# Performance work log

Hardware: AMD Instinct MI355X
Metric: run time of the kernel (lower is better)

Reference implementation:

```python
import jax, jax.numpy as jnp
import numpy as np

K = 8          # opt.pk, explicit precision cutoff
MARGIN = 0.2   # opt.margin
NEG = -1e30    # sentinel for masked sort keys


def setup_inputs() -> dict:
    key = jax.random.key(0)
    k1, k2 = jax.random.split(key)
    batch_reprs = jax.random.normal(k1, (4096, 512), dtype=jnp.float32)
    batch_labels = jax.random.randint(k2, (4096,), 0, 64)
    return {"batch_reprs": batch_reprs, "batch_labels": batch_labels}


def _forward(batch_reprs, batch_labels):
    B = batch_reprs.shape[0]
    dt = batch_reprs.dtype
    # cls_match_mat: 1 if same class
    match = (batch_labels[:, None] == batch_labels[None, :]).astype(dt)
    # pairwise euclidean distance (squared=False), safe sqrt at zero diagonal
    sq = jnp.sum(batch_reprs * batch_reprs, axis=1)
    res = jnp.maximum(sq[:, None] - 2.0 * (batch_reprs @ batch_reprs.T) + sq[None, :], 0.0)
    zero = res <= 0.0
    d = jnp.where(zero, 0.0, jnp.sqrt(jnp.where(zero, 1.0, res)))
    sim_hat = -d + (1.0 - match) * MARGIN  # use_margin=True path
    # rank via double argsort (descending similarity -> rank 1 = best)
    order = jnp.argsort(-sim_hat, axis=1)
    rank = jnp.argsort(order, axis=1).astype(dt) + 1.0
    pos_nums = jnp.sum(match, axis=1)
    ks = jnp.minimum(pos_nums, jnp.asarray(K + 1, dt))[:, None]  # k_mat per row
    w = 1.0 / jnp.log2(rank + 1.0) + 1.0  # DCG-style rank weight
    # false positives: not same class, within top-k_i
    fp_mask = (match < 1.0) & (rank <= ks)
    fp_nums = jnp.sum(fp_mask, axis=1)  # |N| per row
    # false negatives: same class, beyond top-k_i
    fn_mask = (match > 0.0) & (rank > ks)
    fp_term = jnp.sum(jnp.where(fp_mask, sim_hat * w, 0.0))
    # per-row variable-size topk over false negatives, vectorized:
    # mask non-FN entries to -inf, sort desc, keep first fp_nums[i] entries
    fn_key = jnp.where(fn_mask, sim_hat, NEG)
    fn_order = jnp.argsort(-fn_key, axis=1)
    sorted_sim = jnp.take_along_axis(sim_hat, fn_order, axis=1)
    sorted_w = jnp.take_along_axis(w, fn_order, axis=1)
    sorted_valid = jnp.take_along_axis(fn_mask, fn_order, axis=1)
    take = (jnp.arange(B)[None, :].astype(dt) < fp_nums[:, None]) & sorted_valid
    fn_term = jnp.sum(jnp.where(take, sorted_sim * sorted_w, 0.0))
    # rows with fp_num==0 contribute 0 to both terms, matching the host loop
    return fp_term - fn_term


def reference(batch_reprs, batch_labels):
    return _forward(batch_reprs, batch_labels)
```

## Files before the change

kernel.cpp:

```cpp
#include <hip/hip_runtime.h>
#include <math.h>

#define BB 4096
#define DD 512
#define KTOP 9
#define MARGIN_F 0.2f
#define NT64 64
#define NTRI64 (NT64 * (NT64 + 1) / 2)

typedef __attribute__((ext_vector_type(8))) short short8;
typedef __attribute__((ext_vector_type(4))) float f32x4;
typedef unsigned long long u64;

__device__ unsigned short g_Rhi[(size_t)BB * DD];
__device__ u64 g_cmask[64 * 64];

__device__ __forceinline__ unsigned short f2bf(float x) {
  unsigned u = __float_as_uint(x);
  u += 0x7fffu + ((u >> 16) & 1u);
  return (unsigned short)(u >> 16);
}

__device__ __forceinline__ void gload16(void* lds, const void* g) {
  __builtin_amdgcn_global_load_lds(
      (const __attribute__((address_space(1))) void*)g,
      (__attribute__((address_space(3))) void*)lds, 16, 0, 0);
}

__device__ __forceinline__ float ord16val(unsigned o16) {
  unsigned e = (o16 << 16) | 0x8000u;
  unsigned s = (e & 0x80000000u) ? (e ^ 0x80000000u) : ~e;
  return __uint_as_float(s);
}

__device__ __forceinline__ unsigned wavemax32_dpp(unsigned c) {
#define MSTEP(CTRL, RM)                                                        \
  {                                                                            \
    unsigned o = (unsigned)__builtin_amdgcn_update_dpp(0, (int)c, CTRL, RM, 0xf, false); \
    if (o > c) c = o;                                                          \
  }
  MSTEP(0xB1, 0xf) MSTEP(0x4E, 0xf) MSTEP(0x141, 0xf) MSTEP(0x140, 0xf)
  MSTEP(0x142, 0xa) MSTEP(0x143, 0xc)
#undef MSTEP
  return (unsigned)__builtin_amdgcn_readlane((int)c, 63);
}

__device__ __forceinline__ int wavesum_dpp(int c) {
#define SSTEP(CTRL, RM)                                                        \
  c += __builtin_amdgcn_update_dpp(0, c, CTRL, RM, 0xf, false);
  SSTEP(0xB1, 0xf) SSTEP(0x4E, 0xf) SSTEP(0x141, 0xf) SSTEP(0x140, 0xf)
  SSTEP(0x142, 0xa) SSTEP(0x143, 0xc)
#undef SSTEP
  return __builtin_amdgcn_readlane(c, 63);
}

__device__ __forceinline__ unsigned u4c(const uint4& f, int q) {
  return q == 0 ? f.x : q == 1 ? f.y : q == 2 ? f.z : f.w;
}

__global__ __launch_bounds__(64) void splitsq(const float* __restrict__ R,
                                              float* __restrict__ sq) {
  const int row = blockIdx.x, lane = threadIdx.x;
  const float4* r4 = (const float4*)(R + (size_t)row * DD);
  float4 a = r4[lane], b = r4[lane + 64];
  float xs[8] = {a.x, a.y, a.z, a.w, b.x, b.y, b.z, b.w};
  unsigned short hs[8];
  float s = 0.f;
  #pragma unroll
  for (int q = 0; q < 8; ++q) {
    float x = xs[q];
    s += x * x;
    hs[q] = f2bf(x);
  }
  const size_t base = (size_t)row * DD;
  *(ushort4*)&g_Rhi[base + lane * 4]       = *(ushort4*)&hs[0];
  *(ushort4*)&g_Rhi[base + 256 + lane * 4] = *(ushort4*)&hs[4];
  #pragma unroll
  for (int off = 32; off; off >>= 1) s += __shfl_down(s, off);
  if (lane == 0) sq[row] = s;
}

__global__ __launch_bounds__(64) void buildmask(const int* __restrict__ labels) {
  __shared__ int slab[BB];
  const int c = blockIdx.x, lane = threadIdx.x;
  for (int i = lane; i < BB / 4; i += 64) ((int4*)slab)[i] = ((const int4*)labels)[i];
  __syncthreads();
  u64 m = 0;
  #pragma unroll
  for (int e = 0; e < 64; ++e) {
    int j = 512 * (e >> 3) + 8 * lane + (e & 7);
    m |= (u64)(slab[j] == c) << e;
  }
  g_cmask[c * 64 + lane] = m;
}

__global__ __launch_bounds__(64) void simgemm_wave(const int* __restrict__ labels,
                                                   const float* __restrict__ sq,
                                                   unsigned short* __restrict__ simq) {
  const int x = blockIdx.x & 7;
  int c = blockIdx.x >> 3;
  int bi = 0, bj = 0;
  #pragma unroll
  for (int q = 0; q < 8; ++q) {
    const int bjq = (q < 4) ? (4 * x + q) : (56 - 4 * x + q);
    const int n = bjq + 1;
    if (c >= 0 && c < n) { bj = bjq; bi = c; }
    c -= n;
  }
  const int i0 = bi * 64, j0 = bj * 64;

  __shared__ unsigned short smem[2][2][2048];

  const int lane = threadIdx.x;
  const int lrow = lane & 15, kblk = lane >> 4;

  f32x4 acc[4][4] = {};

  auto stage = [&](int buf, int k0) {
    const int sr = lane & 15;
    const int sc = (lane >> 4) * 8;
    #pragma unroll
    for (int m = 0; m < 4; ++m) {
      gload16(&smem[buf][0][m * 512], &g_Rhi[(size_t)(i0 + m * 16 + sr) * DD + k0 + sc]);
      gload16(&smem[buf][1][m * 512], &g_Rhi[(size_t)(j0 + m * 16 + sr) * DD + k0 + sc]);
    }
  };

  stage(0, 0);
  stage(1, 32);

  #pragma unroll
  for (int step = 0; step < 16; ++step) {
    const int cur = step & 1;
    if (step == 15) asm volatile("s_waitcnt vmcnt(0)" ::: "memory");
    else            asm volatile("s_waitcnt vmcnt(8)" ::: "memory");
    __builtin_amdgcn_sched_barrier(0);

    short8 a[4], b[4];
    #pragma unroll
    for (int m = 0; m < 4; ++m) a[m] = *(const short8*)&smem[cur][0][m * 512 + lane * 8];
    #pragma unroll
    for (int n = 0; n < 4; ++n) b[n] = *(const short8*)&smem[cur][1][n * 512 + lane * 8];
    asm volatile("s_waitcnt lgkmcnt(0)" ::: "memory");
    __builtin_amdgcn_sched_barrier(0);

    if (step < 14) stage(cur, (step + 2) * 32);

    #pragma unroll
    for (int m = 0; m < 4; ++m) {
      #pragma unroll
      for (int n = 0; n < 4; ++n) {
        acc[m][n] = __builtin_amdgcn_mfma_f32_16x16x32_bf16(a[m], b[n], acc[m][n], 0, 0, 0);
      }
    }
  }

  unsigned short* flat = &smem[0][0][0];
  unsigned short (*T)[68] = (unsigned short (*)[68])flat;
  float* sqi = (float*)(flat + 4608);
  float* sqj = sqi + 64;
  int* labi = (int*)(sqj + 64);
  int* labj = labi + 64;
  sqi[lane] = sq[i0 + lane];
  sqj[lane] = sq[j0 + lane];
  labi[lane] = labels[i0 + lane];
  labj[lane] = labels[j0 + lane];

  #pragma unroll
  for (int m = 0; m < 4; ++m) {
    const int rbase = m * 16 + kblk * 4;
    #pragma unroll
    for (int n = 0; n < 4; ++n) {
      const int ccol = n * 16 + lrow;
      const float sqc = sqj[ccol];
      const int lc_ = labj[ccol];
      #pragma unroll
      for (int reg = 0; reg < 4; ++reg) {
        const int r = rbase + reg;
        float res = sqi[r] - 2.0f * acc[m][n][reg] + sqc;
        float dd = (res <= 0.f) ? 0.f : sqrtf(res);
        float sv = -dd + ((labi[r] != lc_) ? MARGIN_F : 0.f);
        unsigned su = __float_as_uint(sv);
        unsigned ord = su ^ ((unsigned)((int)su >> 31) | 0x80000000u);
        T[r][ccol] = (unsigned short)(ord >> 16);
      }
    }
  }

  #pragma unroll
  for (int s = 0; s < 8; ++s) {
    const int row = s * 8 + (lane >> 3);
    const int cs = (lane & 7) * 8;
    short8 w = *(const short8*)&T[row][cs];
    *(short8*)&simq[(size_t)(i0 + row) * BB + j0 + cs] = w;
  }
  if (bi != bj) {
    #pragma unroll
    for (int s = 0; s < 8; ++s) {
      const int col = s * 8 + (lane >> 3);
      const int rs = (lane & 7) * 8;
      unsigned short tmp[8];
      #pragma unroll
      for (int t = 0; t < 8; ++t) tmp[t] = T[rs + t][col];
      *(short8*)&simq[(size_t)(j0 + col) * BB + i0 + rs] = *(short8*)tmp;
    }
  }
}

#define EKEY(e) ((((u4c(v[(e) >> 3], ((e) & 7) >> 1) >> (16 * ((e) & 1))) & 0xffffu) << 13) \
                 | (lbase - (unsigned)((512 * ((e) >> 3) + ((e) & 7)) << 1)                 \
                    + (unsigned)((mask >> (e)) & 1ull)))

#define TOP2UPD(k, a, b) {                                                     \
  unsigned _mx = ((k) > (a)) ? (k) : (a);                                      \
  unsigned _mn = ((k) > (a)) ? (a) : (k);                                      \
  (a) = _mx;                                                                   \
  (b) = (_mn > (b)) ? _mn : (b); }

__global__ __launch_bounds__(256) void rowproc6(const unsigned short* __restrict__ simq,
                                                const int* __restrict__ labels,
                                                float* __restrict__ partials) {
  const int tid = threadIdx.x;
  const int lane = tid & 63;
  const int row = blockIdx.x * 4 + (tid >> 6);

  const uint4* rowp = (const uint4*)(simq + (size_t)row * BB);
  uint4 v[8];
  #pragma unroll
  for (int s = 0; s < 8; ++s) v[s] = rowp[lane + s * 64];

  const int myl = labels[row];
  const u64 mask = g_cmask[myl * 64 + lane];
  const unsigned lbase = (unsigned)((4095 - 8 * lane) << 1);

  unsigned h1 = 0, h2 = 0;
  #pragma unroll
  for (int e = 0; e < 64; ++e) {
    unsigned k = EKEY(e);
    TOP2UPD(k, h1, h2);
  }
  const int pos = wavesum_dpp(__popcll(mask));
  const int ks = min(pos, KTOP);

  unsigned kth = 0;
  float fp = 0.f; int fpn = 0;
  #pragma unroll
  for (int t = 0; t < KTOP; ++t) {
    if (t < ks) {
      unsigned g = wavemax32_dpp(h1);
      if (!(g & 1u)) { fp += ord16val(g >> 13) * (1.f / log2f((float)(t + 2)) + 1.f); fpn++; }
      if (t == ks - 1) kth = g;
      if (h1 == g) {
        h1 = h2; h2 = ~0u;
        if (h1 == ~0u) {
          h1 = 0; h2 = 0;
          #pragma unroll
          for (int e = 0; e < 64; ++e) {
            unsigned k = EKEY(e);
            if (k < g) TOP2UPD(k, h1, h2);
          }
        }
      }
    }
  }

  float fn = 0.f;
  if (fpn > 0) {
    unsigned f1 = 0, f2 = 0;
    #pragma unroll
    for (int e = 0; e < 64; ++e) {
      unsigned k = EKEY(e);
      if ((k & 1u) && k < kth) TOP2UPD(k, f1, f2);
    }
    unsigned ck[KTOP];
    int nc = 0;
    #pragma unroll
    for (int u = 0; u < KTOP; ++u) {
      ck[u] = ~0u;
      if (u < fpn) {
        unsigned g = wavemax32_dpp(f1);
        if (g != 0u) {
          ck[u] = g; nc = u + 1;
          if (f1 == g) {
            f1 = f2; f2 = ~0u;
            if (f1 == ~0u) {
              f1 = 0; f2 = 0;
              #pragma unroll
              for (int e = 0; e < 64; ++e) {
                unsigned k = EKEY(e);
                if ((k & 1u) && k < g) TOP2UPD(k, f1, f2);
              }
            }
          }
        }
      }
    }
    if (nc > 0) {
      int cnt[KTOP];
      #pragma unroll
      for (int u = 0; u < KTOP; ++u) cnt[u] = 0;
      #pragma unroll
      for (int e = 0; e < 64; ++e) {
        unsigned k = EKEY(e);
        #pragma unroll
        for (int u = 0; u < KTOP; ++u) cnt[u] += (k > ck[u]) ? 1 : 0;
      }
      #pragma unroll
      for (int u = 0; u < KTOP; ++u) cnt[u] = wavesum_dpp(cnt[u]);
      #pragma unroll
      for (int u = 0; u < KTOP; ++u) {
        if (u < nc) {
          int rank = 1 + cnt[u];
          fn += ord16val(ck[u] >> 13) * (1.f / log2f((float)(rank + 1)) + 1.f);
        }
      }
    }
  }

  if (lane == 0) partials[row] = fp - fn;
}

__global__ __launch_bounds__(256) void finalreduce(const float* __restrict__ partials,
                                                   float* __restrict__ out) {
  __shared__ float s[256];
  const int tid = threadIdx.x;
  float acc = 0.f;
  for (int j = tid; j < BB; j += 256) acc += partials[j];
  s[tid] = acc; __syncthreads();
  #pragma unroll
  for (int st = 128; st; st >>= 1) { if (tid < st) s[tid] += s[tid + st]; __syncthreads(); }
  if (tid == 0) out[0] = s[0];
}

extern "C" void kernel_launch(void* const* d_in, const int* in_sizes, int n_in,
                              void* d_out, int out_size, void* d_ws, size_t ws_size,
                              hipStream_t stream) {
  const float* R      = (const float*)d_in[0];
  const int*   labels = (const int*)d_in[1];
  float* out = (float*)d_out;

  unsigned short* simq = (unsigned short*)d_ws;
  float* sq            = (float*)((char*)d_ws + (size_t)BB * BB * 2);
  float* partials      = sq + BB;

  splitsq<<<BB, 64, 0, stream>>>(R, sq);
  buildmask<<<64, 64, 0, stream>>>(labels);
  simgemm_wave<<<NTRI64, 64, 0, stream>>>(labels, sq, simq);
  rowproc6<<<BB / 4, 256, 0, stream>>>(simq, labels, partials);
  finalreduce<<<1, 256, 0, stream>>>(partials, out);
}
```

Before: 96.12 us.

## Use 128x128 four-wave tiles for the similarity GEMM to increase operand reuse

Replaces the single-wave 64x64 triangular GEMM tiles with 256-thread blocks computing 128x128 tiles. Each wave computes a 64x64 quadrant from shared LDS A/B buffers, so each global load is reused by two waves. The grid shrinks from 2080 to 528 blocks. The hand-tuned vmcnt waits are replaced by __syncthreads with a single-stage prefetch, which can expose load latency and leaves fewer blocks to fill the GPU.

```diff
diff --git a/kernel.cpp b/kernel.cpp
--- a/kernel.cpp
+++ b/kernel.cpp
@@ -5,8 +5,8 @@
 #define DD 512
 #define KTOP 9
 #define MARGIN_F 0.2f
-#define NT64 64
-#define NTRI64 (NT64 * (NT64 + 1) / 2)
+#define NT 32
+#define NTRI (NT * (NT + 1) / 2)
 
 typedef __attribute__((ext_vector_type(8))) short short8;
 typedef __attribute__((ext_vector_type(4))) float f32x4;
@@ -94,24 +94,27 @@
   g_cmask[c * 64 + lane] = m;
 }
 
-__global__ __launch_bounds__(64) void simgemm_wave(const int* __restrict__ labels,
-                                                   const float* __restrict__ sq,
-                                                   unsigned short* __restrict__ simq) {
+__global__ __launch_bounds__(256) void simgemm_mfma2(const int* __restrict__ labels,
+                                                     const float* __restrict__ sq,
+                                                     unsigned short* __restrict__ simq) {
   const int x = blockIdx.x & 7;
   int c = blockIdx.x >> 3;
   int bi = 0, bj = 0;
   #pragma unroll
-  for (int q = 0; q < 8; ++q) {
-    const int bjq = (q < 4) ? (4 * x + q) : (56 - 4 * x + q);
+  for (int q = 0; q < 4; ++q) {
+    const int bjq = (q < 2) ? (2 * x + q) : (28 - 2 * x + q);
     const int n = bjq + 1;
     if (c >= 0 && c < n) { bj = bjq; bi = c; }
     c -= n;
   }
-  const int i0 = bi * 64, j0 = bj * 64;
-
-  __shared__ unsigned short smem[2][2][2048];
-
-  const int lane = threadIdx.x;
+  const int i0 = bi * 128, j0 = bj * 128;
+
+  __shared__ __align__(16) unsigned char smembytes[35840];
+  unsigned short (*kbuf)[2][4096] = (unsigned short (*)[2][4096])smembytes;
+
+  const int tid = threadIdx.x;
+  const int wid = tid >> 6, lane = tid & 63;
+  const int wr = wid >> 1, wc = wid & 1;
   const int lrow = lane & 15, kblk = lane >> 4;
 
   f32x4 acc[4][4] = {};
@@ -120,31 +123,28 @@
     const int sr = lane & 15;
     const int sc = (lane >> 4) * 8;
     #pragma unroll
-    for (int m = 0; m < 4; ++m) {
-      gload16(&smem[buf][0][m * 512], &g_Rhi[(size_t)(i0 + m * 16 + sr) * DD + k0 + sc]);
-      gload16(&smem[buf][1][m * 512], &g_Rhi[(size_t)(j0 + m * 16 + sr) * DD + k0 + sc]);
+    for (int i = 0; i < 2; ++i) {
+      const int chunk = 2 * wid + i;
+      const int r = chunk * 16 + sr;
+      gload16(&kbuf[buf][0][chunk * 512], &g_Rhi[(size_t)(i0 + r) * DD + k0 + sc]);
+      gload16(&kbuf[buf][1][chunk * 512], &g_Rhi[(size_t)(j0 + r) * DD + k0 + sc]);
     }
   };
 
   stage(0, 0);
-  stage(1, 32);
-
-  #pragma unroll
+
   for (int step = 0; step < 16; ++step) {
     const int cur = step & 1;
-    if (step == 15) asm volatile("s_waitcnt vmcnt(0)" ::: "memory");
-    else            asm volatile("s_waitcnt vmcnt(8)" ::: "memory");
-    __builtin_amdgcn_sched_barrier(0);
+    __syncthreads();
+    if (step < 15) stage(cur ^ 1, (step + 1) * 32);
 
     short8 a[4], b[4];
     #pragma unroll
-    for (int m = 0; m < 4; ++m) a[m] = *(const short8*)&smem[cur][0][m * 512 + lane * 8];
-    #pragma unroll
-    for (int n = 0; n < 4; ++n) b[n] = *(const short8*)&smem[cur][1][n * 512 + lane * 8];
-    asm volatile("s_waitcnt lgkmcnt(0)" ::: "memory");
-    __builtin_amdgcn_sched_barrier(0);
-
-    if (step < 14) stage(cur, (step + 2) * 32);
+    for (int m = 0; m < 4; ++m)
+      a[m] = *(const short8*)&kbuf[cur][0][(wr * 4 + m) * 512 + lane * 8];
+    #pragma unroll
+    for (int n = 0; n < 4; ++n)
+      b[n] = *(const short8*)&kbuf[cur][1][(wc * 4 + n) * 512 + lane * 8];
 
     #pragma unroll
     for (int m = 0; m < 4; ++m) {
@@ -155,23 +155,22 @@
     }
   }
 
-  unsigned short* flat = &smem[0][0][0];
-  unsigned short (*T)[68] = (unsigned short (*)[68])flat;
-  float* sqi = (float*)(flat + 4608);
-  float* sqj = sqi + 64;
-  int* labi = (int*)(sqj + 64);
-  int* labj = labi + 64;
-  sqi[lane] = sq[i0 + lane];
-  sqj[lane] = sq[j0 + lane];
-  labi[lane] = labels[i0 + lane];
-  labj[lane] = labels[j0 + lane];
+  __syncthreads();
+  unsigned short (*T)[132] = (unsigned short (*)[132])smembytes;
+  float* sqi = (float*)(smembytes + 33792);
+  float* sqj = (float*)(smembytes + 34304);
+  int* labi  = (int*)(smembytes + 34816);
+  int* labj  = (int*)(smembytes + 35328);
+  if (tid < 128) { sqi[tid] = sq[i0 + tid]; labi[tid] = labels[i0 + tid]; }
+  else { int t2 = tid - 128; sqj[t2] = sq[j0 + t2]; labj[t2] = labels[j0 + t2]; }
+  __syncthreads();
 
   #pragma unroll
   for (int m = 0; m < 4; ++m) {
-    const int rbase = m * 16 + kblk * 4;
+    const int rbase = wr * 64 + m * 16 + kblk * 4;
     #pragma unroll
     for (int n = 0; n < 4; ++n) {
-      const int ccol = n * 16 + lrow;
+      const int ccol = wc * 64 + n * 16 + lrow;
       const float sqc = sqj[ccol];
       const int lc_ = labj[ccol];
       #pragma unroll
@@ -186,23 +185,23 @@
       }
     }
   }
-
-  #pragma unroll
-  for (int s = 0; s < 8; ++s) {
-    const int row = s * 8 + (lane >> 3);
-    const int cs = (lane & 7) * 8;
-    short8 w = *(const short8*)&T[row][cs];
-    *(short8*)&simq[(size_t)(i0 + row) * BB + j0 + cs] = w;
+  __syncthreads();
+
+  const int srow0 = tid >> 4, scol0 = (tid & 15) * 8;
+  #pragma unroll
+  for (int p = 0; p < 8; ++p) {
+    const int r = p * 16 + srow0;
+    short8 w = *(const short8*)&T[r][scol0];
+    *(short8*)&simq[(size_t)(i0 + r) * BB + j0 + scol0] = w;
   }
   if (bi != bj) {
     #pragma unroll
-    for (int s = 0; s < 8; ++s) {
-      const int col = s * 8 + (lane >> 3);
-      const int rs = (lane & 7) * 8;
+    for (int p = 0; p < 8; ++p) {
+      const int col = p * 16 + srow0;
       unsigned short tmp[8];
       #pragma unroll
-      for (int t = 0; t < 8; ++t) tmp[t] = T[rs + t][col];
-      *(short8*)&simq[(size_t)(j0 + col) * BB + i0 + rs] = *(short8*)tmp;
+      for (int t = 0; t < 8; ++t) tmp[t] = T[scol0 + t][col];
+      *(short8*)&simq[(size_t)(j0 + col) * BB + i0 + scol0] = *(short8*)tmp;
     }
   }
 }
@@ -345,7 +344,7 @@
 
   splitsq<<<BB, 64, 0, stream>>>(R, sq);
   buildmask<<<64, 64, 0, stream>>>(labels);
-  simgemm_wave<<<NTRI64, 64, 0, stream>>>(labels, sq, simq);
+  simgemm_mfma2<<<NTRI, 256, 0, stream>>>(labels, sq, simq);
   rowproc6<<<BB / 4, 256, 0, stream>>>(simq, labels, partials);
   finalreduce<<<1, 256, 0, stream>>>(partials, out);
 }
```

Result: slower. 98.19 us (+2.2%).
